# Kernel tuning notes

Hardware: AMD Instinct MI355X
Metric: run time of the kernel (lower is better)

Reference implementation:

```python
import jax, jax.numpy as jnp
import numpy as np

EPS_BN = 1e-4


def gcn_conv(x, W, b, src, dst):
    """PyG GCNConv with added self-loops and symmetric normalization."""
    N = x.shape[0]
    h = x @ W  # [N, out]
    # degree over targets, +1 for the implicit self-loop on every node
    deg = jnp.zeros((N,), x.dtype).at[dst].add(1.0) + 1.0
    dinv = jax.lax.rsqrt(deg)  # deg^{-1/2}
    norm = dinv[src] * dinv[dst]  # per-edge coefficient
    msg = h[src] * norm[:, None]  # [E, out] gather (memory-bound)
    out = jax.ops.segment_sum(msg, dst, num_segments=N)
    out = out + h * (dinv * dinv)[:, None]  # self-loop term, norm = 1/deg
    return out + b


def batch_norm(x, gamma, beta):
    # training-mode BN over the node dim, biased variance (matches torch train)
    m = jnp.mean(x, axis=0)
    v = jnp.mean(jnp.square(x - m), axis=0)
    return (x - m) * jax.lax.rsqrt(v + EPS_BN) * gamma + beta


def setup_inputs() -> dict:
    key = jax.random.key(0)
    ks = jax.random.split(key, 8)
    N, E, D = 100000, 1600000, 64
    L = 2
    x = jax.random.normal(ks[0], (N, D), jnp.float32)
    edge_index = jax.random.randint(ks[1], (2, E), 0, N, jnp.int32)
    batch = jnp.sort(jax.random.randint(ks[2], (N,), 0, 128, jnp.int32))
    s = 1.0 / np.sqrt(D)
    return {
        "x": x,
        "edge_index": edge_index,
        "batch": batch,
        "enc_W": jax.random.normal(ks[3], (L, D, D), jnp.float32) * s,
        "enc_b": jnp.zeros((L, D), jnp.float32),
        "enc_gamma": jnp.ones((L, D), jnp.float32),
        "enc_beta": jnp.zeros((L, D), jnp.float32),
        "attr_W": jax.random.normal(ks[4], (L, D, D), jnp.float32) * s,
        "attr_b": jnp.zeros((L, D), jnp.float32),
        "attr_gamma": jnp.ones((L, D), jnp.float32),
        "attr_beta": jnp.zeros((L, D), jnp.float32),
        "str_W": jax.random.normal(ks[5], (L, D, D), jnp.float32) * s,
        "str_b": jnp.zeros((L, D), jnp.float32),
        "str_gamma": jnp.ones((L, D), jnp.float32),
        "str_beta": jnp.zeros((L, D), jnp.float32),
    }


def reference(x, edge_index, batch, enc_W, enc_b, enc_gamma, enc_beta,
              attr_W, attr_b, attr_gamma, attr_beta,
              str_W, str_b, str_gamma, str_beta):
    src, dst = edge_index[0], edge_index[1]
    L = enc_W.shape[0]

    # ---- Encoder: GCN -> sigmoid -> (dropout id) -> BN ----
    h = x
    for i in range(L):
        h = gcn_conv(h, enc_W[i], enc_b[i], src, dst)
        h = jax.nn.sigmoid(h)
        h = batch_norm(h, enc_gamma[i], enc_beta[i])
    x_enc = h
    # x_pool = global_mean_pool(x_enc, batch) is computed but discarded upstream

    # ---- Attribute decoder: GCN -> (dropout) -> sigmoid (except last) -> BN ----
    h = x_enc
    for i in range(L):
        h = gcn_conv(h, attr_W[i], attr_b[i], src, dst)
        if i != L - 1:
            h = jax.nn.sigmoid(h)
        h = batch_norm(h, attr_gamma[i], attr_beta[i])
    x_att = h

    # ---- Structure decoder ----
    h = x_enc
    for i in range(L):
        h = gcn_conv(h, str_W[i], str_b[i], src, dst)
        if i != L - 1:
            h = jax.nn.sigmoid(h)
        else:
            h = jax.nn.sigmoid(h * 0.5)
        h = batch_norm(h, str_gamma[i], str_beta[i])
    x_str = h

    return (x_str, x_att, x_enc)
```

## Files before the change

kernel.cpp:

```cpp
#include <hip/hip_runtime.h>

#define D 64
#define BCH 4096

typedef __attribute__((ext_vector_type(8))) _Float16 f16x8;
typedef __attribute__((ext_vector_type(4))) float f32x4;

__device__ __forceinline__ float sigmoidf_(float x) {
    return 1.0f / (1.0f + __expf(-x));
}
__device__ __forceinline__ float h2f(ushort u) {
    _Float16 h;
    __builtin_memcpy(&h, &u, 2);
    return (float)h;
}
__device__ __forceinline__ ushort f2h(float f) {
    _Float16 h = (_Float16)f;
    ushort u;
    __builtin_memcpy(&u, &h, 2);
    return u;
}
__device__ __forceinline__ float2 up2(uint v) {
    float2 r;
    r.x = h2f((ushort)(v & 0xffffu));
    r.y = h2f((ushort)(v >> 16));
    return r;
}


__global__ __launch_bounds__(256) void bin_edges(const int* __restrict__ src,
                                                 const int* __restrict__ dst,
                                                 int* __restrict__ bcur,
                                                 uint* __restrict__ bins,
                                                 int CAP, int E) {
    __shared__ uint lp[BCH];
    __shared__ unsigned char lb[BCH];
    __shared__ int hist[128], base[128];
    int t = threadIdx.x;
    int e0 = blockIdx.x * BCH;
    if (t < 128) hist[t] = 0;
    __syncthreads();
    for (int k = t; k < BCH; k += 256) {
        int e = e0 + k;
        uint p = 0xFFFFFFFFu;
        int b = 0;
        if (e < E) {
            int s_ = src[e];
            int d_ = dst[e];
            b = d_ >> 10;
            atomicAdd(&hist[b], 1);
            p = ((uint)s_ << 10) | (uint)(d_ & 1023);
        }
        lp[k] = p;
        lb[k] = (unsigned char)b;
    }
    __syncthreads();
    if (t < 128) {
        int c = hist[t];
        base[t] = (c > 0) ? atomicAdd(&bcur[t], c) : 0;
        hist[t] = 0;
    }
    __syncthreads();
    for (int k = t; k < BCH; k += 256) {
        uint p = lp[k];
        if (p != 0xFFFFFFFFu) {
            int b = lb[k];
            int pos = base[b] + atomicAdd(&hist[b], 1);
            bins[(size_t)b * CAP + pos] = p;
        }
    }
}

__global__ __launch_bounds__(128) void scan_nb(const int* __restrict__ bcur,
                                               int* __restrict__ boff,
                                               int* __restrict__ csr,
                                               int NB, int N, int E) {
    __shared__ int tmp[128];
    int t = threadIdx.x;
    int v = (t < NB) ? bcur[t] : 0;
    tmp[t] = v;
    __syncthreads();
    for (int o = 1; o < 128; o <<= 1) {
        int x = (t >= o) ? tmp[t - o] : 0;
        __syncthreads();
        tmp[t] += x;
        __syncthreads();
    }
    if (t < NB) boff[t] = tmp[t] - v;
    if (t == 0) csr[N] = E;
}

__global__ __launch_bounds__(256) void build_csr(const uint* __restrict__ bins,
                                                 const int* __restrict__ bcur,
                                                 const int* __restrict__ boff,
                                                 int* __restrict__ csr,
                                                 int* __restrict__ sorted,
                                                 float* __restrict__ dinv,
                                                 float* __restrict__ rdinv,
                                                 int CAP, int N) {
    __shared__ int hist[1024];
    __shared__ int part[256];
    int t = threadIdx.x;
    int b = blockIdx.x;
    int nb0 = b << 10;
    int cnt = bcur[b];
    int e0 = boff[b];
    const uint* bp = bins + (size_t)b * CAP;
    for (int k = t; k < 1024; k += 256) hist[k] = 0;
    __syncthreads();
    for (int k = t; k < cnt; k += 256) atomicAdd(&hist[bp[k] & 1023u], 1);
    __syncthreads();
    int v0 = hist[4 * t], v1 = hist[4 * t + 1], v2 = hist[4 * t + 2], v3 = hist[4 * t + 3];
    part[t] = v0 + v1 + v2 + v3;
    __syncthreads();
    for (int o = 1; o < 256; o <<= 1) {
        int x = (t >= o) ? part[t - o] : 0;
        __syncthreads();
        part[t] += x;
        __syncthreads();
    }
    int run = (t > 0) ? part[t - 1] : 0;
    int pre[4];
    pre[0] = run;
    pre[1] = run + v0;
    pre[2] = run + v0 + v1;
    pre[3] = run + v0 + v1 + v2;
    int deg[4] = {v0, v1, v2, v3};
    __syncthreads();
    hist[4 * t + 0] = e0 + pre[0];
    hist[4 * t + 1] = e0 + pre[1];
    hist[4 * t + 2] = e0 + pre[2];
    hist[4 * t + 3] = e0 + pre[3];
#pragma unroll
    for (int j = 0; j < 4; j++) {
        int node = nb0 + 4 * t + j;
        if (node < N) {
            csr[node] = e0 + pre[j];
            float c = (float)deg[j] + 1.0f;
            dinv[node] = rsqrtf(c);
            rdinv[node] = sqrtf(c);
        }
    }
    __syncthreads();
    for (int k = t; k < cnt; k += 256) {
        uint p = bp[k];
        int pos = atomicAdd(&hist[p & 1023u], 1);
        sorted[pos] = (int)(p >> 10);
    }
}


__global__ __launch_bounds__(256) void prep_xd(const float* __restrict__ x,
                                               const float* __restrict__ dinv,
                                               ushort* __restrict__ actd, int N16) {
    int p = blockIdx.x * 256 + threadIdx.x;
    if (p >= N16) return;
    int n = p >> 4;
    float d = dinv[n];
    float4 v = reinterpret_cast<const float4*>(x)[p];
    ushort4 o;
    o.x = f2h(v.x * d);
    o.y = f2h(v.y * d);
    o.z = f2h(v.z * d);
    o.w = f2h(v.w * d);
    reinterpret_cast<ushort4*>(actd)[p] = o;
}

__global__ __launch_bounds__(256) void wprep(const float* __restrict__ W,
                                             ushort* __restrict__ wfrag) {
    int idx = blockIdx.x * 256 + threadIdx.x;
    if (idx >= 4096) return;
    int i = idx & 7;
    int lane = (idx >> 3) & 63;
    int hc = idx >> 9;
    int h = hc >> 2, c = hc & 3;
    int k = h * 32 + (lane >> 4) * 8 + i;
    int j = c * 16 + (lane & 15);
    wfrag[idx] = f2h(W[k * 64 + j]);
}

__global__ __launch_bounds__(256) void layer_prep(const float* __restrict__ ssum,
                                                  const float* __restrict__ sssq,
                                                  const float* __restrict__ gamma,
                                                  const float* __restrict__ beta,
                                                  const float* __restrict__ W,
                                                  float* __restrict__ A,
                                                  float* __restrict__ C,
                                                  float* __restrict__ u,
                                                  ushort* __restrict__ wfrag,
                                                  float invN) {
    __shared__ float As[64], Cs[64];
    int t = threadIdx.x;
    if (t < 64) {
        float m = ssum[t] * invN;
        float var = sssq[t] * invN - m * m;
        float rs = rsqrtf(var + 1e-4f);
        float a = rs * gamma[t];
        As[t] = a;
        A[t] = a;
        float c = fmaf(-m, a, beta[t]);
        Cs[t] = c;
        C[t] = c;
    }
    __syncthreads();
    if (t < 64) {
        float s = 0.f;
        for (int k = 0; k < 64; k++) s = fmaf(Cs[k], W[k * 64 + t], s);
        u[t] = s;
    }
    for (int idx = t; idx < 4096; idx += 256) {
        int i = idx & 7;
        int lane = (idx >> 3) & 63;
        int hc = idx >> 9;
        int h = hc >> 2, c = hc & 3;
        int k = h * 32 + (lane >> 4) * 8 + i;
        int j = c * 16 + (lane & 15);
        wfrag[idx] = f2h(W[k * 64 + j] * As[k]);
    }
}

__global__ __launch_bounds__(64) void finalize_aff(const float* __restrict__ ssum,
                                                   const float* __restrict__ sssq,
                                                   const float* __restrict__ gamma,
                                                   const float* __restrict__ beta,
                                                   float* __restrict__ A,
                                                   float* __restrict__ C, float invN) {
    int c = threadIdx.x;
    float m = ssum[c] * invN;
    float var = sssq[c] * invN - m * m;
    float rs = rsqrtf(var + 1e-4f);
    float a = rs * gamma[c];
    A[c] = a;
    C[c] = fmaf(-m, a, beta[c]);
}


__global__ __launch_bounds__(256) void agg_g(const ushort* __restrict__ actd,
                                             const int* __restrict__ ptr,
                                             const int* __restrict__ srcs,
                                             const float* __restrict__ dinv,
                                             const float* __restrict__ rdinv,
                                             ushort* __restrict__ zh,
                                             float* __restrict__ ssum,
                                             float* __restrict__ sssq,
                                             float* __restrict__ qout, int N, int E) {
    __shared__ float red[2][4][64];
    int lane = threadIdx.x & 63;
    int wv = threadIdx.x >> 6;
    int l7 = lane & 7;
    int Em1 = E - 1;
    const bool do_stats = (ssum != nullptr);
    const bool do_q = (qout != nullptr);
    float ps = 0.f, pq = 0.f;
    int Nh = (N + 1) >> 1;
    for (int n0 = blockIdx.x * 4 + wv; n0 < Nh; n0 += gridDim.x * 4) {
        int nA = n0;
        int nB = n0 + Nh;
        bool hasB = nB < N;
        int sA = ptr[nA], eA = ptr[nA + 1];
        int sB = 0, eB = 0;
        if (hasB) { sB = ptr[nB]; eB = ptr[nB + 1]; }
        float selfA = h2f(actd[((size_t)nA << 6) + lane]);
        float accA = selfA;
        float dnA = dinv[nA];
        float accB = 0.f, dnB = 0.f;
        if (hasB) {
            float selfB = h2f(actd[((size_t)nB << 6) + lane]);
            accB = selfB;
            dnB = dinv[nB];
            if (do_stats) {
                float rb = rdinv[nB];
                float b = selfB * rb;
                ps += b;
                pq += b * b;
            }
        }
        if (do_stats) {
            float ra = rdinv[nA];
            float a = selfA * ra;
            ps += a;
            pq += a * a;
        }
        float qaA = 0.f, qaB = 0.f;
        int iA = sA, iB = sB;
        int idxA = srcs[min(iA + l7, Em1)];
        int idxB = hasB ? srcs[min(iB + l7, Em1)] : 0;
        while (iA + 8 <= eA || iB + 8 <= eB) {
            bool gA = iA + 8 <= eA;
            bool gB = iB + 8 <= eB;
            ushort ua[8], ub[8];
            if (gA) {
#pragma unroll
                for (int j = 0; j < 8; j++) {
                    int u = __builtin_amdgcn_readlane(idxA, j);
                    ua[j] = actd[((size_t)u << 6) + lane];
                    if (do_q) qaA += dinv[u];
                }
            }
            if (gB) {
#pragma unroll
                for (int j = 0; j < 8; j++) {
                    int u = __builtin_amdgcn_readlane(idxB, j);
                    ub[j] = actd[((size_t)u << 6) + lane];
                    if (do_q) qaB += dinv[u];
                }
            }
            int idxA2 = idxA, idxB2 = idxB;
            if (gA) idxA2 = srcs[min(iA + 8 + l7, Em1)];
            if (gB) idxB2 = srcs[min(iB + 8 + l7, Em1)];
            if (gA) {
                accA += ((h2f(ua[0]) + h2f(ua[1])) + (h2f(ua[2]) + h2f(ua[3]))) +
                        ((h2f(ua[4]) + h2f(ua[5])) + (h2f(ua[6]) + h2f(ua[7])));
                iA += 8;
                idxA = idxA2;
            }
            if (gB) {
                accB += ((h2f(ub[0]) + h2f(ub[1])) + (h2f(ub[2]) + h2f(ub[3]))) +
                        ((h2f(ub[4]) + h2f(ub[5])) + (h2f(ub[6]) + h2f(ub[7])));
                iB += 8;
                idxB = idxB2;
            }
        }
        if (iA < eA) {
#pragma unroll
            for (int j = 0; j < 8; j++) {
                int u = __builtin_amdgcn_readlane(idxA, j);
                float w = (iA + j < eA) ? 1.0f : 0.0f;
                float f = h2f(actd[((size_t)u << 6) + lane]);
                accA = fmaf(w, f, accA);
                if (do_q) qaA = fmaf(w, dinv[u], qaA);
            }
        }
        if (hasB && iB < eB) {
#pragma unroll
            for (int j = 0; j < 8; j++) {
                int u = __builtin_amdgcn_readlane(idxB, j);
                float w = (iB + j < eB) ? 1.0f : 0.0f;
                float f = h2f(actd[((size_t)u << 6) + lane]);
                accB = fmaf(w, f, accB);
                if (do_q) qaB = fmaf(w, dinv[u], qaB);
            }
        }
        if (do_q && lane == 0) {
            qout[nA] = dnA * (dnA + qaA);
            if (hasB) qout[nB] = dnB * (dnB + qaB);
        }
        zh[((size_t)nA << 6) + lane] = f2h(accA * dnA);
        if (hasB) zh[((size_t)nB << 6) + lane] = f2h(accB * dnB);
    }
    if (do_stats) {
        red[0][wv][lane] = ps;
        red[1][wv][lane] = pq;
        __syncthreads();
        if (wv == 0) {
            float t0 = red[0][0][lane] + red[0][1][lane] + red[0][2][lane] + red[0][3][lane];
            float t1 = red[1][0][lane] + red[1][1][lane] + red[1][2][lane] + red[1][3][lane];
            atomicAdd(&ssum[lane], t0);
            atomicAdd(&sssq[lane], t1);
        }
    }
}

__global__ __launch_bounds__(256) void agg_dual(const ushort* __restrict__ ab,
                                                const int* __restrict__ ptr,
                                                const int* __restrict__ srcs,
                                                const float* __restrict__ dinv,
                                                const float* __restrict__ rdinv,
                                                ushort* __restrict__ zab,
                                                float* __restrict__ ssA,
                                                float* __restrict__ sqA,
                                                float* __restrict__ ssS,
                                                float* __restrict__ sqS,
                                                int N, int E) {
    __shared__ float red[2][4][128];
    int lane = threadIdx.x & 63;
    int wv = threadIdx.x >> 6;
    int l7 = lane & 7;
    int Em1 = E - 1;
    float2 ps = make_float2(0.f, 0.f), pq = make_float2(0.f, 0.f);
    for (int n = blockIdx.x * 4 + wv; n < N; n += gridDim.x * 4) {
        int s = ptr[n], e = ptr[n + 1];
        uint su = *reinterpret_cast<const uint*>(ab + ((size_t)n << 7) + (lane << 1));
        float2 acc = up2(su);
        {
            float r = rdinv[n];
            float ax = acc.x * r, ay = acc.y * r;
            ps.x += ax; ps.y += ay;
            pq.x += ax * ax; pq.y += ay * ay;
        }
        int i = s;
        int idx8 = srcs[min(i + l7, Em1)];
        while (i + 8 <= e) {
            int ni = i + 8;
            int nidx = srcs[min(ni + l7, Em1)];
#pragma unroll
            for (int j = 0; j < 8; j++) {
                int u = __builtin_amdgcn_readlane(idx8, j);
                uint v = *reinterpret_cast<const uint*>(ab + ((size_t)u << 7) + (lane << 1));
                float2 f = up2(v);
                acc.x += f.x;
                acc.y += f.y;
            }
            idx8 = nidx;
            i = ni;
        }
        if (i < e) {
#pragma unroll
            for (int j = 0; j < 8; j++) {
                int u = __builtin_amdgcn_readlane(idx8, j);
                uint v = *reinterpret_cast<const uint*>(ab + ((size_t)u << 7) + (lane << 1));
                float w = (i + j < e) ? 1.0f : 0.0f;
                float2 f = up2(v);
                acc.x = fmaf(w, f.x, acc.x);
                acc.y = fmaf(w, f.y, acc.y);
            }
        }
        float dn = dinv[n];
        uint pk = (uint)f2h(acc.x * dn) | ((uint)f2h(acc.y * dn) << 16);
        *reinterpret_cast<uint*>(zab + ((size_t)n << 7) + (lane << 1)) = pk;
    }
    red[0][wv][2 * lane + 0] = ps.x;
    red[0][wv][2 * lane + 1] = ps.y;
    red[1][wv][2 * lane + 0] = pq.x;
    red[1][wv][2 * lane + 1] = pq.y;
    __syncthreads();
    if (wv == 0) {
#pragma unroll
        for (int m0 = 0; m0 < 2; m0++) {
            int m = lane + m0 * 64;
            float t0 = red[0][0][m] + red[0][1][m] + red[0][2][m] + red[0][3][m];
            float t1 = red[1][0][m] + red[1][1][m] + red[1][2][m] + red[1][3][m];
            if (m < 64) {
                atomicAdd(&ssA[m], t0);
                atomicAdd(&sqA[m], t1);
            } else {
                atomicAdd(&ssS[m - 64], t0);
                atomicAdd(&sqS[m - 64], t1);
            }
        }
    }
}

template <int MODE, bool HAS_AFF, int OM>
__global__ __launch_bounds__(256) void gemm_mfma(const ushort* __restrict__ zh, int is,
                                                 const ushort* __restrict__ wfrag,
                                                 const float* __restrict__ bias,
                                                 const float* __restrict__ u,
                                                 const float* __restrict__ q,
                                                 const float* __restrict__ dinv,
                                                 ushort* __restrict__ outh, int os,
                                                 float* __restrict__ s0,
                                                 float* __restrict__ s1, int N) {
    int tid = threadIdx.x;
    int lane = tid & 63;
    int wv = tid >> 6;
    int l15 = lane & 15;
    int lg = lane >> 4;
    int tb = blockIdx.x * 64;

    const ushort* zrow = zh + (size_t)(tb + wv * 16 + l15) * is + (lg << 3);
    f16x8 a0 = *reinterpret_cast<const f16x8*>(zrow);
    f16x8 a1 = *reinterpret_cast<const f16x8*>(zrow + 32);

    const f16x8* wf = reinterpret_cast<const f16x8*>(wfrag) + lane;

    f32x4 acc[4];
#pragma unroll
    for (int c = 0; c < 4; c++) {
        f32x4 t = {0.f, 0.f, 0.f, 0.f};
        t = __builtin_amdgcn_mfma_f32_16x16x32_f16(a0, wf[(0 * 4 + c) * 64], t, 0, 0, 0);
        t = __builtin_amdgcn_mfma_f32_16x16x32_f16(a1, wf[(1 * 4 + c) * 64], t, 0, 0, 0);
        acc[c] = t;
    }

    int rowbase = tb + wv * 16 + lg * 4;
    float qv[4], dv[4];
    bool vld[4];
#pragma unroll
    for (int r = 0; r < 4; r++) {
        int row = rowbase + r;
        vld[r] = row < N;
        qv[r] = (HAS_AFF && vld[r]) ? q[row] : 0.f;
        dv[r] = (OM == 0 && vld[r]) ? dinv[row] : 0.f;
    }
    float sa[4], sq[4];
#pragma unroll
    for (int c = 0; c < 4; c++) { sa[c] = 0.f; sq[c] = 0.f; }

#pragma unroll
    for (int c = 0; c < 4; c++) {
        int col = c * 16 + l15;
        float bcol = bias[col];
        float ucol = HAS_AFF ? u[col] : 0.f;
#pragma unroll
        for (int r = 0; r < 4; r++) {
            if (!vld[r]) continue;
            float o = acc[c][r] + bcol;
            if (HAS_AFF) o = fmaf(qv[r], ucol, o);
            float a = (MODE == 0) ? sigmoidf_(o)
                                  : ((MODE == 1) ? o : sigmoidf_(0.5f * o));
            int row = rowbase + r;
            if (OM == 0) {
                outh[(size_t)row * os + col] = f2h(a * dv[r]);
            } else {
                outh[(size_t)row * os + col] = f2h(a);
                sa[c] += a;
                sq[c] += a * a;
            }
        }
    }

    if (OM == 1) {
        __shared__ float red[2][4][4][16];
#pragma unroll
        for (int c = 0; c < 4; c++) {
            sa[c] += __shfl_xor(sa[c], 16);
            sa[c] += __shfl_xor(sa[c], 32);
            sq[c] += __shfl_xor(sq[c], 16);
            sq[c] += __shfl_xor(sq[c], 32);
        }
        if (lg == 0) {
#pragma unroll
            for (int c = 0; c < 4; c++) {
                red[0][wv][c][l15] = sa[c];
                red[1][wv][c][l15] = sq[c];
            }
        }
        __syncthreads();
        if (wv == 0) {
            int c = lane >> 4, l = lane & 15;
            float t0 = red[0][0][c][l] + red[0][1][c][l] + red[0][2][c][l] + red[0][3][c][l];
            float t1 = red[1][0][c][l] + red[1][1][c][l] + red[1][2][c][l] + red[1][3][c][l];
            atomicAdd(&s0[lane], t0);
            atomicAdd(&s1[lane], t1);
        }
    }
}

__global__ __launch_bounds__(256) void gemm_dual(const ushort* __restrict__ zh,
                                                 const ushort* __restrict__ wfA,
                                                 const ushort* __restrict__ wfS,
                                                 const float* __restrict__ bA,
                                                 const float* __restrict__ bS,
                                                 const float* __restrict__ uA,
                                                 const float* __restrict__ uS,
                                                 const float* __restrict__ q,
                                                 const float* __restrict__ dinv,
                                                 ushort* __restrict__ outAB, int N) {
    int tid = threadIdx.x;
    int lane = tid & 63;
    int wv = tid >> 6;
    int l15 = lane & 15;
    int lg = lane >> 4;
    int tb = blockIdx.x * 64;

    const ushort* zrow = zh + ((size_t)(tb + wv * 16 + l15) << 6) + (lg << 3);
    f16x8 a0 = *reinterpret_cast<const f16x8*>(zrow);
    f16x8 a1 = *reinterpret_cast<const f16x8*>(zrow + 32);

    const f16x8* wa = reinterpret_cast<const f16x8*>(wfA) + lane;
    const f16x8* wsp = reinterpret_cast<const f16x8*>(wfS) + lane;

    f32x4 accA[4], accS[4];
#pragma unroll
    for (int c = 0; c < 4; c++) {
        f32x4 t = {0.f, 0.f, 0.f, 0.f};
        t = __builtin_amdgcn_mfma_f32_16x16x32_f16(a0, wa[(0 * 4 + c) * 64], t, 0, 0, 0);
        t = __builtin_amdgcn_mfma_f32_16x16x32_f16(a1, wa[(1 * 4 + c) * 64], t, 0, 0, 0);
        accA[c] = t;
        f32x4 t2 = {0.f, 0.f, 0.f, 0.f};
        t2 = __builtin_amdgcn_mfma_f32_16x16x32_f16(a0, wsp[(0 * 4 + c) * 64], t2, 0, 0, 0);
        t2 = __builtin_amdgcn_mfma_f32_16x16x32_f16(a1, wsp[(1 * 4 + c) * 64], t2, 0, 0, 0);
        accS[c] = t2;
    }

    int rowbase = tb + wv * 16 + lg * 4;
    float qv[4], dv[4];
    bool vld[4];
#pragma unroll
    for (int r = 0; r < 4; r++) {
        int row = rowbase + r;
        vld[r] = row < N;
        qv[r] = vld[r] ? q[row] : 0.f;
        dv[r] = vld[r] ? dinv[row] : 0.f;
    }
#pragma unroll
    for (int c = 0; c < 4; c++) {
        int col = c * 16 + l15;
        float bcA = bA[col], ucA = uA[col];
        float bcS = bS[col], ucS = uS[col];
#pragma unroll
        for (int r = 0; r < 4; r++) {
            if (!vld[r]) continue;
            int row = rowbase + r;
            float oA = fmaf(qv[r], ucA, accA[c][r] + bcA);
            float oS = fmaf(qv[r], ucS, accS[c][r] + bcS);
            float aA = sigmoidf_(oA);
            float aS = sigmoidf_(oS);
            outAB[((size_t)row << 7) + col] = f2h(aA * dv[r]);
            outAB[((size_t)row << 7) + 64 + col] = f2h(aS * dv[r]);
        }
    }
}

__global__ __launch_bounds__(256) void bn_apply_h(const ushort* __restrict__ actd,
                                                  const float* __restrict__ rdinv,
                                                  const float* __restrict__ A,
                                                  const float* __restrict__ C,
                                                  float* __restrict__ out, int N16) {
    int p = blockIdx.x * 256 + threadIdx.x;
    if (p >= N16) return;
    int n = p >> 4;
    int cb = (p & 15) * 4;
    float r = rdinv[n];
    ushort4 v = reinterpret_cast<const ushort4*>(actd)[p];
    float4 o;
    o.x = fmaf(h2f(v.x) * r, A[cb + 0], C[cb + 0]);
    o.y = fmaf(h2f(v.y) * r, A[cb + 1], C[cb + 1]);
    o.z = fmaf(h2f(v.z) * r, A[cb + 2], C[cb + 2]);
    o.w = fmaf(h2f(v.w) * r, A[cb + 3], C[cb + 3]);
    reinterpret_cast<float4*>(out)[p] = o;
}

__global__ __launch_bounds__(256) void bn_apply_hf(const ushort* __restrict__ acth,
                                                   const float* __restrict__ A,
                                                   const float* __restrict__ C,
                                                   float* __restrict__ out, int N16) {
    int p = blockIdx.x * 256 + threadIdx.x;
    if (p >= N16) return;
    int cb = (p & 15) * 4;
    ushort4 v = reinterpret_cast<const ushort4*>(acth)[p];
    float4 o;
    o.x = fmaf(h2f(v.x), A[cb + 0], C[cb + 0]);
    o.y = fmaf(h2f(v.y), A[cb + 1], C[cb + 1]);
    o.z = fmaf(h2f(v.z), A[cb + 2], C[cb + 2]);
    o.w = fmaf(h2f(v.w), A[cb + 3], C[cb + 3]);
    reinterpret_cast<float4*>(out)[p] = o;
}


extern "C" void kernel_launch(void* const* d_in, const int* in_sizes, int n_in,
                              void* d_out, int out_size, void* d_ws, size_t ws_size,
                              hipStream_t stream) {
    const int N = in_sizes[0] / D;
    const int E = in_sizes[1] / 2;

    const float* x = (const float*)d_in[0];
    const int* ei = (const int*)d_in[1];
    const int* src_in = ei;
    const int* dst_in = ei + E;
    const float* encW = (const float*)d_in[3];
    const float* encb = (const float*)d_in[4];
    const float* encg = (const float*)d_in[5];
    const float* encbe = (const float*)d_in[6];
    const float* attW = (const float*)d_in[7];
    const float* attb = (const float*)d_in[8];
    const float* attg = (const float*)d_in[9];
    const float* attbe = (const float*)d_in[10];
    const float* strW = (const float*)d_in[11];
    const float* strb = (const float*)d_in[12];
    const float* strg = (const float*)d_in[13];
    const float* strbe = (const float*)d_in[14];

    const int NB = (N + 1023) >> 10;
    int CAP = (E + NB - 1) / NB;
    CAP = CAP + CAP / 8 + 256;
    CAP = (CAP + 255) & ~255;

    char* ws = (char*)d_ws;
    size_t off = 0;
    auto alloc = [&](size_t bytes) -> char* {
        char* p = ws + off;
        off += (bytes + 255) & ~(size_t)255;
        return p;
    };
    int* csr = (int*)alloc((size_t)(N + 1) * 4);
    int* bcur = (int*)alloc(128 * 4);
    int* boff = (int*)alloc(128 * 4);
    float* dinv = (float*)alloc((size_t)N * 4);
    float* rdinv = (float*)alloc((size_t)N * 4);
    float* q = (float*)alloc((size_t)N * 4);
    float* stats = (float*)alloc(6 * 128 * 4);
    float* aff = (float*)alloc(6 * 128 * 4);
    float* ubuf = (float*)alloc(6 * 64 * 4);
    ushort* wf = (ushort*)alloc(6 * 4096 * 2);
    int* sorted = (int*)alloc((size_t)E * 4);
    ushort* zh = (ushort*)alloc((size_t)(N + 64) * 64 * 2);
    size_t binbytes = (size_t)NB * CAP * 4;
    size_t zabbytes = (size_t)(N + 64) * 128 * 2;
    char* region = alloc(binbytes > zabbytes ? binbytes : zabbytes);
    uint* bins = (uint*)region;
    ushort* zab = (ushort*)region;
    ushort* hA = (ushort*)alloc((size_t)(N + 64) * 64 * 2);
    ushort* hB = (ushort*)alloc((size_t)(N + 64) * 64 * 2);
    ushort* hAB = (ushort*)alloc((size_t)(N + 64) * 128 * 2);

    float* out_str = (float*)d_out;
    float* out_att = out_str + (size_t)N * D;
    float* out_enc = out_att + (size_t)N * D;

    hipMemsetAsync(bcur, 0, 128 * 4, stream);
    hipMemsetAsync(stats, 0, 6 * 128 * 4, stream);

    int N16 = N * 16;
    int g16 = (N16 + 255) / 256;
    int gT = (N + 63) / 64;
    float invN = 1.0f / (float)N;

    float* A0 = aff + 0 * 128; float* C0 = A0 + 64;
    float* A1 = aff + 1 * 128; float* C1 = A1 + 64;
    float* A2 = aff + 2 * 128; float* C2 = A2 + 64;
    float* A3 = aff + 3 * 128; float* C3 = A3 + 64;
    float* A4 = aff + 4 * 128; float* C4 = A4 + 64;
    float* A5 = aff + 5 * 128; float* C5 = A5 + 64;
    ushort* wf0 = wf + 0 * 4096;
    ushort* wf1 = wf + 1 * 4096;
    ushort* wf2 = wf + 2 * 4096;
    ushort* wf3 = wf + 3 * 4096;
    ushort* wf4 = wf + 4 * 4096;
    ushort* wf5 = wf + 5 * 4096;

    bin_edges<<<(E + BCH - 1) / BCH, 256, 0, stream>>>(src_in, dst_in, bcur,
                                                       bins, CAP, E);
    scan_nb<<<1, 128, 0, stream>>>(bcur, boff, csr, NB, N, E);
    build_csr<<<NB, 256, 0, stream>>>(bins, bcur, boff, csr, sorted,
                                      dinv, rdinv, CAP, N);

    prep_xd<<<g16, 256, 0, stream>>>(x, dinv, hA, N16);
    wprep<<<16, 256, 0, stream>>>(encW, wf0);
    agg_g<<<2048, 256, 0, stream>>>(hA, csr, sorted, dinv, rdinv, zh,
                                    nullptr, nullptr, q, N, E);
    gemm_mfma<0, false, 0><<<gT, 256, 0, stream>>>(zh, 64, wf0, encb, nullptr,
                                                   q, dinv, hB, 64,
                                                   nullptr, nullptr, N);
    agg_g<<<2048, 256, 0, stream>>>(hB, csr, sorted, dinv, rdinv, zh,
                                    stats + 0, stats + 64, nullptr, N, E);
    layer_prep<<<1, 256, 0, stream>>>(stats + 0, stats + 64, encg, encbe,
                                      encW + 4096, A0, C0, ubuf + 0, wf1, invN);
    gemm_mfma<0, true, 0><<<gT, 256, 0, stream>>>(zh, 64, wf1, encb + 64, ubuf + 0,
                                                  q, dinv, hA, 64,
                                                  nullptr, nullptr, N);
    agg_g<<<2048, 256, 0, stream>>>(hA, csr, sorted, dinv, rdinv, zh,
                                    stats + 128, stats + 192, nullptr, N, E);
    layer_prep<<<1, 256, 0, stream>>>(stats + 128, stats + 192, encg + 64,
                                      encbe + 64, attW, A1, C1, ubuf + 64, wf2, invN);
    layer_prep<<<1, 256, 0, stream>>>(stats + 128, stats + 192, encg + 64,
                                      encbe + 64, strW, A1, C1, ubuf + 128, wf3, invN);
    bn_apply_h<<<g16, 256, 0, stream>>>(hA, rdinv, A1, C1, out_enc, N16);
    gemm_dual<<<gT, 256, 0, stream>>>(zh, wf2, wf3, attb, strb, ubuf + 64,
                                      ubuf + 128, q, dinv, hAB, N);
    agg_dual<<<2048, 256, 0, stream>>>(hAB, csr, sorted, dinv, rdinv, zab,
                                       stats + 256, stats + 320,
                                       stats + 512, stats + 576, N, E);
    layer_prep<<<1, 256, 0, stream>>>(stats + 256, stats + 320, attg, attbe,
                                      attW + 4096, A2, C2, ubuf + 192, wf4, invN);
    gemm_mfma<1, true, 1><<<gT, 256, 0, stream>>>(zab, 128, wf4, attb + 64,
                                                  ubuf + 192, q, dinv, hAB, 64,
                                                  stats + 384, stats + 448, N);
    finalize_aff<<<1, 64, 0, stream>>>(stats + 384, stats + 448, attg + 64,
                                       attbe + 64, A3, C3, invN);
    bn_apply_hf<<<g16, 256, 0, stream>>>(hAB, A3, C3, out_att, N16);
    layer_prep<<<1, 256, 0, stream>>>(stats + 512, stats + 576, strg, strbe,
                                      strW + 4096, A4, C4, ubuf + 320, wf5, invN);
    gemm_mfma<2, true, 1><<<gT, 256, 0, stream>>>(zab + 64, 128, wf5, strb + 64,
                                                  ubuf + 320, q, dinv, hA, 64,
                                                  stats + 640, stats + 704, N);
    finalize_aff<<<1, 64, 0, stream>>>(stats + 640, stats + 704, strg + 64,
                                       strbe + 64, A5, C5, invN);
    bn_apply_hf<<<g16, 256, 0, stream>>>(hA, A5, C5, out_str, N16);
}
```

Baseline: 595.3 us.

## Fold BN affine prep into consumer kernels and batch weight-fragment prep

Removes the single-block layer_prep and finalize_aff launches. Each GEMM and bn_apply block now recomputes the BN scale and shift from the raw stats, and the GEMM kernels recompute the C·W bias vector. The BN scale is applied to the A operand in fp16 instead of being folded into the weight fragments. All six weight-fragment conversions are done up front in one wprep6 launch, cutting about seven tiny serial launches. The cost is redundant per-block prologue work, extra syncthreads, and slightly different rounding from scaling activations in fp16.

```diff
diff --git a/kernel.cpp b/kernel.cpp
--- a/kernel.cpp
+++ b/kernel.cpp
@@ -166,72 +166,25 @@
     reinterpret_cast<ushort4*>(actd)[p] = o;
 }
 
-__global__ __launch_bounds__(256) void wprep(const float* __restrict__ W,
-                                             ushort* __restrict__ wfrag) {
-    int idx = blockIdx.x * 256 + threadIdx.x;
-    if (idx >= 4096) return;
+__global__ __launch_bounds__(256) void wprep6(const float* __restrict__ encW,
+                                              const float* __restrict__ attW,
+                                              const float* __restrict__ strW,
+                                              ushort* __restrict__ wf) {
+    int w = blockIdx.x >> 4;
+    int idx = (blockIdx.x & 15) * 256 + threadIdx.x;
+    const float* W = (w == 0) ? encW
+                   : (w == 1) ? (encW + 4096)
+                   : (w == 2) ? attW
+                   : (w == 3) ? strW
+                   : (w == 4) ? (attW + 4096)
+                              : (strW + 4096);
     int i = idx & 7;
     int lane = (idx >> 3) & 63;
     int hc = idx >> 9;
     int h = hc >> 2, c = hc & 3;
     int k = h * 32 + (lane >> 4) * 8 + i;
     int j = c * 16 + (lane & 15);
-    wfrag[idx] = f2h(W[k * 64 + j]);
-}
-
-__global__ __launch_bounds__(256) void layer_prep(const float* __restrict__ ssum,
-                                                  const float* __restrict__ sssq,
-                                                  const float* __restrict__ gamma,
-                                                  const float* __restrict__ beta,
-                                                  const float* __restrict__ W,
-                                                  float* __restrict__ A,
-                                                  float* __restrict__ C,
-                                                  float* __restrict__ u,
-                                                  ushort* __restrict__ wfrag,
-                                                  float invN) {
-    __shared__ float As[64], Cs[64];
-    int t = threadIdx.x;
-    if (t < 64) {
-        float m = ssum[t] * invN;
-        float var = sssq[t] * invN - m * m;
-        float rs = rsqrtf(var + 1e-4f);
-        float a = rs * gamma[t];
-        As[t] = a;
-        A[t] = a;
-        float c = fmaf(-m, a, beta[t]);
-        Cs[t] = c;
-        C[t] = c;
-    }
-    __syncthreads();
-    if (t < 64) {
-        float s = 0.f;
-        for (int k = 0; k < 64; k++) s = fmaf(Cs[k], W[k * 64 + t], s);
-        u[t] = s;
-    }
-    for (int idx = t; idx < 4096; idx += 256) {
-        int i = idx & 7;
-        int lane = (idx >> 3) & 63;
-        int hc = idx >> 9;
-        int h = hc >> 2, c = hc & 3;
-        int k = h * 32 + (lane >> 4) * 8 + i;
-        int j = c * 16 + (lane & 15);
-        wfrag[idx] = f2h(W[k * 64 + j] * As[k]);
-    }
-}
-
-__global__ __launch_bounds__(64) void finalize_aff(const float* __restrict__ ssum,
-                                                   const float* __restrict__ sssq,
-                                                   const float* __restrict__ gamma,
-                                                   const float* __restrict__ beta,
-                                                   float* __restrict__ A,
-                                                   float* __restrict__ C, float invN) {
-    int c = threadIdx.x;
-    float m = ssum[c] * invN;
-    float var = sssq[c] * invN - m * m;
-    float rs = rsqrtf(var + 1e-4f);
-    float a = rs * gamma[c];
-    A[c] = a;
-    C[c] = fmaf(-m, a, beta[c]);
+    wf[w * 4096 + idx] = f2h(W[k * 64 + j]);
 }
 
 
@@ -444,13 +397,20 @@
 template <int MODE, bool HAS_AFF, int OM>
 __global__ __launch_bounds__(256) void gemm_mfma(const ushort* __restrict__ zh, int is,
                                                  const ushort* __restrict__ wfrag,
+                                                 const float* __restrict__ st0,
+                                                 const float* __restrict__ st1,
+                                                 const float* __restrict__ gamma,
+                                                 const float* __restrict__ beta,
+                                                 const float* __restrict__ Wf32,
                                                  const float* __restrict__ bias,
-                                                 const float* __restrict__ u,
                                                  const float* __restrict__ q,
                                                  const float* __restrict__ dinv,
                                                  ushort* __restrict__ outh, int os,
-                                                 float* __restrict__ s0,
-                                                 float* __restrict__ s1, int N) {
+                                                 float* __restrict__ so0,
+                                                 float* __restrict__ so1,
+                                                 float invN, int N) {
+    __shared__ float Cs[64], us[64];
+    __shared__ ushort aph[64];
     int tid = threadIdx.x;
     int lane = tid & 63;
     int wv = tid >> 6;
@@ -458,9 +418,32 @@
     int lg = lane >> 4;
     int tb = blockIdx.x * 64;
 
+    if (HAS_AFF) {
+        if (tid < 64) {
+            float m = st0[tid] * invN;
+            float var = st1[tid] * invN - m * m;
+            float a = rsqrtf(var + 1e-4f) * gamma[tid];
+            Cs[tid] = fmaf(-m, a, beta[tid]);
+            aph[tid] = f2h(a);
+        }
+        __syncthreads();
+        if (tid < 64) {
+            float s = 0.f;
+#pragma unroll
+            for (int k = 0; k < 64; k++) s = fmaf(Cs[k], Wf32[k * 64 + tid], s);
+            us[tid] = s;
+        }
+        __syncthreads();
+    }
+
     const ushort* zrow = zh + (size_t)(tb + wv * 16 + l15) * is + (lg << 3);
     f16x8 a0 = *reinterpret_cast<const f16x8*>(zrow);
     f16x8 a1 = *reinterpret_cast<const f16x8*>(zrow + 32);
+    if (HAS_AFF) {
+        const f16x8* aps = reinterpret_cast<const f16x8*>(aph);
+        a0 = a0 * aps[lg];
+        a1 = a1 * aps[4 + lg];
+    }
 
     const f16x8* wf = reinterpret_cast<const f16x8*>(wfrag) + lane;
 
@@ -491,7 +474,7 @@
     for (int c = 0; c < 4; c++) {
         int col = c * 16 + l15;
         float bcol = bias[col];
-        float ucol = HAS_AFF ? u[col] : 0.f;
+        float ucol = HAS_AFF ? us[col] : 0.f;
 #pragma unroll
         for (int r = 0; r < 4; r++) {
             if (!vld[r]) continue;
@@ -531,8 +514,8 @@
             int c = lane >> 4, l = lane & 15;
             float t0 = red[0][0][c][l] + red[0][1][c][l] + red[0][2][c][l] + red[0][3][c][l];
             float t1 = red[1][0][c][l] + red[1][1][c][l] + red[1][2][c][l] + red[1][3][c][l];
-            atomicAdd(&s0[lane], t0);
-            atomicAdd(&s1[lane], t1);
+            atomicAdd(&so0[lane], t0);
+            atomicAdd(&so1[lane], t1);
         }
     }
 }
@@ -540,13 +523,20 @@
 __global__ __launch_bounds__(256) void gemm_dual(const ushort* __restrict__ zh,
                                                  const ushort* __restrict__ wfA,
                                                  const ushort* __restrict__ wfS,
+                                                 const float* __restrict__ st0,
+                                                 const float* __restrict__ st1,
+                                                 const float* __restrict__ gamma,
+                                                 const float* __restrict__ beta,
+                                                 const float* __restrict__ WAf32,
+                                                 const float* __restrict__ WSf32,
                                                  const float* __restrict__ bA,
                                                  const float* __restrict__ bS,
-                                                 const float* __restrict__ uA,
-                                                 const float* __restrict__ uS,
                                                  const float* __restrict__ q,
                                                  const float* __restrict__ dinv,
-                                                 ushort* __restrict__ outAB, int N) {
+                                                 ushort* __restrict__ outAB,
+                                                 float invN, int N) {
+    __shared__ float Cs[64], usA[64], usS[64];
+    __shared__ ushort aph[64];
     int tid = threadIdx.x;
     int lane = tid & 63;
     int wv = tid >> 6;
@@ -554,9 +544,36 @@
     int lg = lane >> 4;
     int tb = blockIdx.x * 64;
 
+    if (tid < 64) {
+        float m = st0[tid] * invN;
+        float var = st1[tid] * invN - m * m;
+        float a = rsqrtf(var + 1e-4f) * gamma[tid];
+        Cs[tid] = fmaf(-m, a, beta[tid]);
+        aph[tid] = f2h(a);
+    }
+    __syncthreads();
+    if (tid < 64) {
+        float s = 0.f;
+#pragma unroll
+        for (int k = 0; k < 64; k++) s = fmaf(Cs[k], WAf32[k * 64 + tid], s);
+        usA[tid] = s;
+    } else if (tid < 128) {
+        int j = tid - 64;
+        float s = 0.f;
+#pragma unroll
+        for (int k = 0; k < 64; k++) s = fmaf(Cs[k], WSf32[k * 64 + j], s);
+        usS[j] = s;
+    }
+    __syncthreads();
+
     const ushort* zrow = zh + ((size_t)(tb + wv * 16 + l15) << 6) + (lg << 3);
     f16x8 a0 = *reinterpret_cast<const f16x8*>(zrow);
     f16x8 a1 = *reinterpret_cast<const f16x8*>(zrow + 32);
+    {
+        const f16x8* aps = reinterpret_cast<const f16x8*>(aph);
+        a0 = a0 * aps[lg];
+        a1 = a1 * aps[4 + lg];
+    }
 
     const f16x8* wa = reinterpret_cast<const f16x8*>(wfA) + lane;
     const f16x8* wsp = reinterpret_cast<const f16x8*>(wfS) + lane;
@@ -587,8 +604,8 @@
 #pragma unroll
     for (int c = 0; c < 4; c++) {
         int col = c * 16 + l15;
-        float bcA = bA[col], ucA = uA[col];
-        float bcS = bS[col], ucS = uS[col];
+        float bcA = bA[col], ucA = usA[col];
+        float bcS = bS[col], ucS = usS[col];
 #pragma unroll
         for (int r = 0; r < 4; r++) {
             if (!vld[r]) continue;
@@ -605,36 +622,62 @@
 
 __global__ __launch_bounds__(256) void bn_apply_h(const ushort* __restrict__ actd,
                                                   const float* __restrict__ rdinv,
-                                                  const float* __restrict__ A,
-                                                  const float* __restrict__ C,
-                                                  float* __restrict__ out, int N16) {
-    int p = blockIdx.x * 256 + threadIdx.x;
+                                                  const float* __restrict__ st0,
+                                                  const float* __restrict__ st1,
+                                                  const float* __restrict__ gamma,
+                                                  const float* __restrict__ beta,
+                                                  float* __restrict__ out,
+                                                  float invN, int N16) {
+    __shared__ float As[64], Cs[64];
+    int t = threadIdx.x;
+    if (t < 64) {
+        float m = st0[t] * invN;
+        float var = st1[t] * invN - m * m;
+        float a = rsqrtf(var + 1e-4f) * gamma[t];
+        As[t] = a;
+        Cs[t] = fmaf(-m, a, beta[t]);
+    }
+    __syncthreads();
+    int p = blockIdx.x * 256 + t;
     if (p >= N16) return;
     int n = p >> 4;
     int cb = (p & 15) * 4;
     float r = rdinv[n];
     ushort4 v = reinterpret_cast<const ushort4*>(actd)[p];
     float4 o;
-    o.x = fmaf(h2f(v.x) * r, A[cb + 0], C[cb + 0]);
-    o.y = fmaf(h2f(v.y) * r, A[cb + 1], C[cb + 1]);
-    o.z = fmaf(h2f(v.z) * r, A[cb + 2], C[cb + 2]);
-    o.w = fmaf(h2f(v.w) * r, A[cb + 3], C[cb + 3]);
+    o.x = fmaf(h2f(v.x) * r, As[cb + 0], Cs[cb + 0]);
+    o.y = fmaf(h2f(v.y) * r, As[cb + 1], Cs[cb + 1]);
+    o.z = fmaf(h2f(v.z) * r, As[cb + 2], Cs[cb + 2]);
+    o.w = fmaf(h2f(v.w) * r, As[cb + 3], Cs[cb + 3]);
     reinterpret_cast<float4*>(out)[p] = o;
 }
 
 __global__ __launch_bounds__(256) void bn_apply_hf(const ushort* __restrict__ acth,
-                                                   const float* __restrict__ A,
-                                                   const float* __restrict__ C,
-                                                   float* __restrict__ out, int N16) {
-    int p = blockIdx.x * 256 + threadIdx.x;
+                                                   const float* __restrict__ st0,
+                                                   const float* __restrict__ st1,
+                                                   const float* __restrict__ gamma,
+                                                   const float* __restrict__ beta,
+                                                   float* __restrict__ out,
+                                                   float invN, int N16) {
+    __shared__ float As[64], Cs[64];
+    int t = threadIdx.x;
+    if (t < 64) {
+        float m = st0[t] * invN;
+        float var = st1[t] * invN - m * m;
+        float a = rsqrtf(var + 1e-4f) * gamma[t];
+        As[t] = a;
+        Cs[t] = fmaf(-m, a, beta[t]);
+    }
+    __syncthreads();
+    int p = blockIdx.x * 256 + t;
     if (p >= N16) return;
     int cb = (p & 15) * 4;
     ushort4 v = reinterpret_cast<const ushort4*>(acth)[p];
     float4 o;
-    o.x = fmaf(h2f(v.x), A[cb + 0], C[cb + 0]);
-    o.y = fmaf(h2f(v.y), A[cb + 1], C[cb + 1]);
-    o.z = fmaf(h2f(v.z), A[cb + 2], C[cb + 2]);
-    o.w = fmaf(h2f(v.w), A[cb + 3], C[cb + 3]);
+    o.x = fmaf(h2f(v.x), As[cb + 0], Cs[cb + 0]);
+    o.y = fmaf(h2f(v.y), As[cb + 1], Cs[cb + 1]);
+    o.z = fmaf(h2f(v.z), As[cb + 2], Cs[cb + 2]);
+    o.w = fmaf(h2f(v.w), As[cb + 3], Cs[cb + 3]);
     reinterpret_cast<float4*>(out)[p] = o;
 }
 
@@ -681,8 +724,6 @@
     float* rdinv = (float*)alloc((size_t)N * 4);
     float* q = (float*)alloc((size_t)N * 4);
     float* stats = (float*)alloc(6 * 128 * 4);
-    float* aff = (float*)alloc(6 * 128 * 4);
-    float* ubuf = (float*)alloc(6 * 64 * 4);
     ushort* wf = (ushort*)alloc(6 * 4096 * 2);
     int* sorted = (int*)alloc((size_t)E * 4);
     ushort* zh = (ushort*)alloc((size_t)(N + 64) * 64 * 2);
@@ -707,12 +748,6 @@
     int gT = (N + 63) / 64;
     float invN = 1.0f / (float)N;
 
-    float* A0 = aff + 0 * 128; float* C0 = A0 + 64;
-    float* A1 = aff + 1 * 128; float* C1 = A1 + 64;
-    float* A2 = aff + 2 * 128; float* C2 = A2 + 64;
-    float* A3 = aff + 3 * 128; float* C3 = A3 + 64;
-    float* A4 = aff + 4 * 128; float* C4 = A4 + 64;
-    float* A5 = aff + 5 * 128; float* C5 = A5 + 64;
     ushort* wf0 = wf + 0 * 4096;
     ushort* wf1 = wf + 1 * 4096;
     ushort* wf2 = wf + 2 * 4096;
@@ -727,45 +762,42 @@
                                       dinv, rdinv, CAP, N);
 
     prep_xd<<<g16, 256, 0, stream>>>(x, dinv, hA, N16);
-    wprep<<<16, 256, 0, stream>>>(encW, wf0);
+    wprep6<<<96, 256, 0, stream>>>(encW, attW, strW, wf);
+
     agg_g<<<2048, 256, 0, stream>>>(hA, csr, sorted, dinv, rdinv, zh,
                                     nullptr, nullptr, q, N, E);
-    gemm_mfma<0, false, 0><<<gT, 256, 0, stream>>>(zh, 64, wf0, encb, nullptr,
-                                                   q, dinv, hB, 64,
-                                                   nullptr, nullptr, N);
+    gemm_mfma<0, false, 0><<<gT, 256, 0, stream>>>(zh, 64, wf0,
+                                                   nullptr, nullptr, nullptr, nullptr,
+                                                   nullptr, encb, q, dinv, hB, 64,
+                                                   nullptr, nullptr, invN, N);
     agg_g<<<2048, 256, 0, stream>>>(hB, csr, sorted, dinv, rdinv, zh,
                                     stats + 0, stats + 64, nullptr, N, E);
-    layer_prep<<<1, 256, 0, stream>>>(stats + 0, stats + 64, encg, encbe,
-                                      encW + 4096, A0, C0, ubuf + 0, wf1, invN);
-    gemm_mfma<0, true, 0><<<gT, 256, 0, stream>>>(zh, 64, wf1, encb + 64, ubuf + 0,
-                                                  q, dinv, hA, 64,
-                                                  nullptr, nullptr, N);
+    gemm_mfma<0, true, 0><<<gT, 256, 0, stream>>>(zh, 64, wf1,
+                                                  stats + 0, stats + 64, encg, encbe,
+                                                  encW + 4096, encb + 64, q, dinv,
+                                                  hA, 64, nullptr, nullptr, invN, N);
     agg_g<<<2048, 256, 0, stream>>>(hA, csr, sorted, dinv, rdinv, zh,
                                     stats + 128, stats + 192, nullptr, N, E);
-    layer_prep<<<1, 256, 0, stream>>>(stats + 128, stats + 192, encg + 64,
-                                      encbe + 64, attW, A1, C1, ubuf + 64, wf2, invN);
-    layer_prep<<<1, 256, 0, stream>>>(stats + 128, stats + 192, encg + 64,
-                                      encbe + 64, strW, A1, C1, ubuf + 128, wf3, invN);
-    bn_apply_h<<<g16, 256, 0, stream>>>(hA, rdinv, A1, C1, out_enc, N16);
-    gemm_dual<<<gT, 256, 0, stream>>>(zh, wf2, wf3, attb, strb, ubuf + 64,
-                                      ubuf + 128, q, dinv, hAB, N);
+    bn_apply_h<<<g16, 256, 0, stream>>>(hA, rdinv, stats + 128, stats + 192,
+                                        encg + 64, encbe + 64, out_enc, invN, N16);
+    gemm_dual<<<gT, 256, 0, stream>>>(zh, wf2, wf3, stats + 128, stats + 192,
+                                      encg + 64, encbe + 64, attW, strW,
+                                      attb, strb, q, dinv, hAB, invN, N);
     agg_dual<<<2048, 256, 0, stream>>>(hAB, csr, sorted, dinv, rdinv, zab,
                                        stats + 256, stats + 320,
                                        stats + 512, stats + 576, N, E);
-    layer_prep<<<1, 256, 0, stream>>>(stats + 256, stats + 320, attg, attbe,
-                                      attW + 4096, A2, C2, ubuf + 192, wf4, invN);
-    gemm_mfma<1, true, 1><<<gT, 256, 0, stream>>>(zab, 128, wf4, attb + 64,
-                                                  ubuf + 192, q, dinv, hAB, 64,
-                                                  stats + 384, stats + 448, N);
-    finalize_aff<<<1, 64, 0, stream>>>(stats + 384, stats + 448, attg + 64,
-                                       attbe + 64, A3, C3, invN);
-    bn_apply_hf<<<g16, 256, 0, stream>>>(hAB, A3, C3, out_att, N16);
-    layer_prep<<<1, 256, 0, stream>>>(stats + 512, stats + 576, strg, strbe,
-                                      strW + 4096, A4, C4, ubuf + 320, wf5, invN);
-    gemm_mfma<2, true, 1><<<gT, 256, 0, stream>>>(zab + 64, 128, wf5, strb + 64,
-                                                  ubuf + 320, q, dinv, hA, 64,
-                                                  stats + 640, stats + 704, N);
-    finalize_aff<<<1, 64, 0, stream>>>(stats + 640, stats + 704, strg + 64,
-                                       strbe + 64, A5, C5, invN);
-    bn_apply_hf<<<g16, 256, 0, stream>>>(hA, A5, C5, out_str, N16);
-}
+    gemm_mfma<1, true, 1><<<gT, 256, 0, stream>>>(zab, 128, wf4,
+                                                  stats + 256, stats + 320, attg, attbe,
+                                                  attW + 4096, attb + 64, q, dinv,
+                                                  hAB, 64, stats + 384, stats + 448,
+                                                  invN, N);
+    bn_apply_hf<<<g16, 256, 0, stream>>>(hAB, stats + 384, stats + 448,
+                                         attg + 64, attbe + 64, out_att, invN, N16);
+    gemm_mfma<2, true, 1><<<gT, 256, 0, stream>>>(zab + 64, 128, wf5,
+                                                  stats + 512, stats + 576, strg, strbe,
+                                                  strW + 4096, strb + 64, q, dinv,
+                                                  hA, 64, stats + 640, stats + 704,
+                                                  invN, N);
+    bn_apply_hf<<<g16, 256, 0, stream>>>(hA, stats + 640, stats + 704,
+                                         strg + 64, strbe + 64, out_str, invN, N16);
+}
```

Measured after the change: 585.7 us. No clear change (-1.6%).
